# Kernel optimization log

Measured on AMD Instinct MI355X. Metric: run time of the kernel, lower is better.

## Reference

```python
import jax, jax.numpy as jnp
import numpy as np

N_NODES = 100000
D = 128


def gcn_conv(x, W, b, src, dst, deg_inv_sqrt):
    # PyG GCNConv: linear transform, symmetric-normalized aggregation with self-loops, bias
    h = x @ W  # [N, D_out]
    norm = deg_inv_sqrt[src] * deg_inv_sqrt[dst]  # [E_tot]
    msgs = h[src] * norm[:, None]  # gather + scale  [E_tot, D_out]
    out = jax.ops.segment_sum(msgs, dst, num_segments=x.shape[0])  # scatter-add to targets
    return out + b


def _prep_edges(edge_index, n_nodes):
    # add self-loops (weight 1) and compute deg^{-1/2} over targets (flow source_to_target)
    loops = jnp.arange(n_nodes, dtype=edge_index.dtype)
    src = jnp.concatenate([edge_index[0], loops])
    dst = jnp.concatenate([edge_index[1], loops])
    deg = jax.ops.segment_sum(jnp.ones_like(dst, dtype=jnp.float32), dst, num_segments=n_nodes)
    deg_inv_sqrt = jnp.where(deg > 0, jax.lax.rsqrt(jnp.maximum(deg, 1.0)), 0.0)
    return src, dst, deg_inv_sqrt


def setup_inputs() -> dict:
    key = jax.random.key(0)
    ks = jax.random.split(key, 8)
    node_fts = jax.random.normal(ks[0], (N_NODES, D), dtype=jnp.float32)
    edge_index = jax.random.randint(ks[1], (2, 1600000), 0, N_NODES, dtype=jnp.int64)
    scale = 1.0 / np.sqrt(D)
    W1 = jax.random.uniform(ks[2], (D, D), jnp.float32, -scale, scale)
    b1 = jnp.zeros((D,), jnp.float32)
    W2 = jax.random.uniform(ks[3], (D, D), jnp.float32, -scale, scale)
    b2 = jnp.zeros((D,), jnp.float32)
    W3 = jax.random.uniform(ks[4], (D, D), jnp.float32, -scale, scale)
    b3 = jnp.zeros((D,), jnp.float32)
    return {"node_fts": node_fts, "edge_index": edge_index,
            "W1": W1, "b1": b1, "W2": W2, "b2": b2, "W3": W3, "b3": b3}


def reference(node_fts, edge_index, W1, b1, W2, b2, W3, b3):
    n = node_fts.shape[0]
    src, dst, dinv = _prep_edges(edge_index, n)
    x = jax.nn.relu(gcn_conv(node_fts, W1, b1, src, dst, dinv))
    x = jax.nn.relu(gcn_conv(x, W2, b2, src, dst, dinv))
    x = jax.nn.relu(gcn_conv(x, W3, b3, src, dst, dinv))
    return x
```

## Files before the change

kernel.cpp:

```cpp
#include <hip/hip_runtime.h>

#define NN 100000
#define EE 1600000
#define NPART 8
#define PSZ (NN / NPART)
#define NI4 (EE / 4)
#define SUBW 196
#define NSB (NPART * 64)
#define SCAP 4096
#define RCAP 8192
#define LBCAP 96
#define ROWCAP 64
#define WTB 48

typedef __attribute__((ext_vector_type(8))) short bf16x8;
typedef __attribute__((ext_vector_type(4))) float f32x4;

__device__ inline unsigned int f2bf2(float a, float b) {
    unsigned int ua = __float_as_uint(a);
    unsigned int ub = __float_as_uint(b);
    ua = (ua + 0x7fffu + ((ua >> 16) & 1u)) >> 16;
    ub = (ub + 0x7fffu + ((ub >> 16) & 1u)) >> 16;
    return ua | (ub << 16);
}
__device__ inline unsigned short f2bf(float a) {
    unsigned int u = __float_as_uint(a);
    return (unsigned short)((u + 0x7fffu + ((u >> 16) & 1u)) >> 16);
}
__device__ inline float2 bf2f2(unsigned int u) {
    return make_float2(__uint_as_float(u << 16), __uint_as_float(u & 0xffff0000u));
}


__global__ __launch_bounds__(256) void fbwt_kernel(const int4* __restrict__ src4,
                                                   const int4* __restrict__ dst4,
                                                   int* __restrict__ gcur2,
                                                   uint2* __restrict__ buckets2,
                                                   const float* __restrict__ W1,
                                                   const float* __restrict__ W2,
                                                   const float* __restrict__ W3,
                                                   unsigned short* __restrict__ wt1,
                                                   unsigned short* __restrict__ wt2,
                                                   unsigned short* __restrict__ wt3,
                                                   unsigned int* __restrict__ hb,
                                                   float* __restrict__ dinv) {
    __shared__ uint2 bins[64][LBCAP];
    __shared__ int bcnt[64];
    __shared__ int gbase[64];
    __shared__ float tile[32][33];
    const int bx = blockIdx.x;

    if (bx < WTB) {
        const int m = bx >> 4;
        const int tl = bx & 15;
        const int ti = tl >> 2, tj = tl & 3;
        const float* W = m == 0 ? W1 : (m == 1 ? W2 : W3);
        unsigned short* wt = m == 0 ? wt1 : (m == 1 ? wt2 : wt3);
        const int r = threadIdx.x >> 5, c = threadIdx.x & 31;
#pragma unroll
        for (int rr = r; rr < 32; rr += 8)
            tile[rr][c] = W[(ti * 32 + rr) * 128 + tj * 32 + c];
        __syncthreads();
#pragma unroll
        for (int rr = r; rr < 32; rr += 8)
            wt[(size_t)(tj * 32 + rr) * 128 + ti * 32 + c] = f2bf(tile[c][rr]);
        if (bx == 0) {
            if (threadIdx.x < 64) hb[(size_t)NN * 64 + threadIdx.x] = 0;
            if (threadIdx.x == 64) dinv[NN] = 0.0f;
        }
        return;
    }

    const int fb = bx - WTB;
    const int p = fb >> 6;
    const int c = fb & 63;
    if (threadIdx.x < 64) bcnt[threadIdx.x] = 0;
    __syncthreads();
    const int lo = p * PSZ, hi = lo + PSZ;
    const int chunk4 = NI4 / 64;
    const int a0 = c * chunk4, a1 = a0 + chunk4;
    for (int i = a0 + threadIdx.x; i < a1; i += 256) {
        int4 d4 = dst4[i];
        bool m0 = (d4.x >= lo && d4.x < hi);
        bool m1 = (d4.y >= lo && d4.y < hi);
        bool m2 = (d4.z >= lo && d4.z < hi);
        bool m3 = (d4.w >= lo && d4.w < hi);
        if (!(m0 | m1 | m2 | m3)) continue;
        int4 s4 = src4[i];
        int ss[4] = {s4.x, s4.y, s4.z, s4.w};
        int dd[4] = {d4.x, d4.y, d4.z, d4.w};
        bool mm[4] = {m0, m1, m2, m3};
#pragma unroll
        for (int k = 0; k < 4; ++k) {
            if (!mm[k]) continue;
            int li = (dd[k] - lo) / SUBW;
            int pos = atomicAdd(&bcnt[li], 1);
            if (pos < LBCAP) {
                bins[li][pos] = make_uint2((unsigned)ss[k], (unsigned)dd[k]);
            } else {
                int sb = p * 64 + li;
                int gp = atomicAdd(&gcur2[sb], 1);
                buckets2[(size_t)sb * SCAP + gp] = make_uint2((unsigned)ss[k], (unsigned)dd[k]);
            }
        }
    }
    __syncthreads();
    if (threadIdx.x < 64) {
        int cc = min(bcnt[threadIdx.x], LBCAP);
        gbase[threadIdx.x] = atomicAdd(&gcur2[p * 64 + threadIdx.x], cc);
        bcnt[threadIdx.x] = cc;
    }
    __syncthreads();
    for (int b = 0; b < 64; ++b) {
        const int cc = bcnt[b];
        uint2* outp = buckets2 + (size_t)(p * 64 + b) * SCAP + gbase[b];
        for (int i = threadIdx.x; i < cc; i += 256) outp[i] = bins[b][i];
    }
}


template <bool F32IN>
__device__ __forceinline__ void gemm_body(int wave, const void* __restrict__ xin,
                                          const unsigned short* __restrict__ wt,
                                          unsigned int* __restrict__ hb) {
    const int base = wave * 64;
    if (base >= NN) return;
    const int lane = threadIdx.x & 63;
    const int r = lane & 15;
    const int q = lane >> 4;
    const unsigned short* wrow = wt + (size_t)r * 128 + q * 8;
    bf16x8 wfr[4][8];
#pragma unroll
    for (int kc = 0; kc < 4; ++kc)
#pragma unroll
        for (int nt = 0; nt < 8; ++nt)
            wfr[kc][nt] = *(const bf16x8*)(wrow + (size_t)nt * 16 * 128 + kc * 32);
#pragma unroll
    for (int tt = 0; tt < 4; ++tt) {
        const int m0 = base + tt * 16;
        if (m0 >= NN) break;
        f32x4 acc[8] = {};
#pragma unroll
        for (int kc = 0; kc < 4; ++kc) {
            bf16x8 xf;
            if (F32IN) {
                const float* xrow = (const float*)xin + (size_t)(m0 + r) * 128 + q * 8 + kc * 32;
                float4 a = *(const float4*)xrow;
                float4 b = *(const float4*)(xrow + 4);
                unsigned short tmp[8] = {f2bf(a.x), f2bf(a.y), f2bf(a.z), f2bf(a.w),
                                         f2bf(b.x), f2bf(b.y), f2bf(b.z), f2bf(b.w)};
                xf = *(const bf16x8*)tmp;
            } else {
                const unsigned short* xrow =
                    (const unsigned short*)xin + (size_t)(m0 + r) * 128 + q * 8 + kc * 32;
                xf = *(const bf16x8*)xrow;
            }
#pragma unroll
            for (int nt = 0; nt < 8; ++nt)
                acc[nt] = __builtin_amdgcn_mfma_f32_16x16x32_bf16(wfr[kc][nt], xf, acc[nt], 0, 0, 0);
        }
        const int orow = m0 + r;
        unsigned int* hrow = hb + (size_t)orow * 64;
#pragma unroll
        for (int nt = 0; nt < 8; ++nt) {
            int n = nt * 16 + q * 4;
            *(uint2*)(hrow + (n >> 1)) =
                make_uint2(f2bf2(acc[nt][0], acc[nt][1]), f2bf2(acc[nt][2], acc[nt][3]));
        }
    }
}


__global__ __launch_bounds__(256, 2) void sort3_gemm1_kernel(const uint2* __restrict__ buckets2,
                                                             const int* __restrict__ gcur2,
                                                             int* __restrict__ csr,
                                                             int* __restrict__ deg,
                                                             float* __restrict__ dinv,
                                                             const float* __restrict__ x0,
                                                             const unsigned short* __restrict__ wt1,
                                                             unsigned int* __restrict__ hb) {
    __shared__ int hist[256];
    __shared__ int pscan[256];
    __shared__ int lcur[256];
    __shared__ int rs[256];
    __shared__ int staged[RCAP];
    if (blockIdx.x >= 512) {
        const int wave = (blockIdx.x - 512) * 4 + (threadIdx.x >> 6);
        gemm_body<true>(wave, (const void*)x0, wt1, hb);
        return;
    }
    const int sb = blockIdx.x;
    const int li = sb & 63;
    const int base_node = (sb >> 6) * PSZ + li * SUBW;
    const int nnodes = min(SUBW, PSZ - li * SUBW);
    const int scnt = gcur2[sb];
    const uint2* bk = buckets2 + (size_t)sb * SCAP;
    const int t = threadIdx.x;
    hist[t] = 0;
    __syncthreads();
    for (int i = t; i < scnt; i += 256) atomicAdd(&hist[(int)bk[i].y - base_node], 1);
    __syncthreads();
    const int padded = (t < nnodes) ? ((hist[t] + 7) & ~7) : 0;
    pscan[t] = padded;
    __syncthreads();
    for (int off = 1; off < 256; off <<= 1) {
        int v = (t >= off) ? pscan[t - off] : 0;
        __syncthreads();
        pscan[t] += v;
        __syncthreads();
    }
    const int rstart = pscan[t] - padded;
    lcur[t] = rstart;
    rs[t] = rstart;
    __syncthreads();
    const int total = pscan[255];
    for (int i = t; i < total; i += 256) staged[i] = NN;
    __syncthreads();
    for (int i = t; i < scnt; i += 256) {
        uint2 r = bk[i];
        int pos = atomicAdd(&lcur[(int)r.y - base_node], 1);
        staged[pos] = (int)r.x;
    }
    __syncthreads();
    const int4* staged4 = (const int4*)staged;
    int4* csr4 = (int4*)csr;
    const int4 sv = make_int4(NN, NN, NN, NN);
    for (int i = t; i < nnodes * 16; i += 256) {
        const int n = i >> 4, s = i & 15;
        const int pad = (hist[n] + 7) & ~7;
        int4 v = (s * 4 < pad) ? staged4[(rs[n] >> 2) + s] : sv;
        csr4[((size_t)(base_node + n) << 4) + s] = v;
    }
    if (t < nnodes) {
        int dg = hist[t];
        deg[base_node + t] = dg;
        dinv[base_node + t] = rsqrtf(1.0f + (float)dg);
    }
}

template <bool F32IN>
__global__ __launch_bounds__(256, 2) void gemm_kernel(const void* __restrict__ xin,
                                                      const unsigned short* __restrict__ wt,
                                                      unsigned int* __restrict__ hb) {
    const int wave = blockIdx.x * 4 + (threadIdx.x >> 6);
    gemm_body<F32IN>(wave, xin, wt, hb);
}


#define GATH4(c, v0, v1, v2, v3, w0, w1, w2, w3)                              \
    unsigned int v0 = hb[(size_t)(c).x * 64 + j], v1 = hb[(size_t)(c).y * 64 + j], \
                 v2 = hb[(size_t)(c).z * 64 + j], v3 = hb[(size_t)(c).w * 64 + j]; \
    float w0 = dinv[(c).x], w1 = dinv[(c).y], w2 = dinv[(c).z], w3 = dinv[(c).w];

#define ACC4(v0, v1, v2, v3, w0, w1, w2, w3)                                  \
    {                                                                         \
        float2 f0 = bf2f2(v0), f1 = bf2f2(v1), f2 = bf2f2(v2), f3 = bf2f2(v3);\
        acc.x += (w0 * f0.x + w1 * f1.x) + (w2 * f2.x + w3 * f3.x);           \
        acc.y += (w0 * f0.y + w1 * f1.y) + (w2 * f2.y + w3 * f3.y);           \
    }

template <bool BF16OUT>
__global__ __launch_bounds__(256) void aggregate_kernel(const unsigned int* __restrict__ hb,
                                                        const int* __restrict__ csr,
                                                        const int* __restrict__ deg,
                                                        const float* __restrict__ dinv,
                                                        const float2* __restrict__ bias2,
                                                        void* __restrict__ outp) {
    const int d = blockIdx.x * 4 + (threadIdx.x >> 6);
    const int j = threadIdx.x & 63;
    const int dg = deg[d];
    const float dv = dinv[d];
    const int4* crow = (const int4*)(csr + ((size_t)d << 6));
    float2 acc;
    {
        float2 s = bf2f2(hb[(size_t)d * 64 + j]);
        acc.x = dv * s.x;
        acc.y = dv * s.y;
    }
    int4 c0 = crow[0], c1 = crow[1], c2 = crow[2], c3 = crow[3];
    int4 c4 = crow[4], c5 = crow[5], c6 = crow[6], c7 = crow[7];
    GATH4(c0, va0, va1, va2, va3, wa0, wa1, wa2, wa3)
    GATH4(c1, vb0, vb1, vb2, vb3, wb0, wb1, wb2, wb3)
    GATH4(c2, vc0, vc1, vc2, vc3, wc0, wc1, wc2, wc3)
    GATH4(c3, vd0, vd1, vd2, vd3, wd0, wd1, wd2, wd3)
    GATH4(c4, ve0, ve1, ve2, ve3, we0, we1, we2, we3)
    GATH4(c5, vf0, vf1, vf2, vf3, wf0, wf1, wf2, wf3)
    GATH4(c6, vg0, vg1, vg2, vg3, wg0, wg1, wg2, wg3)
    GATH4(c7, vh0, vh1, vh2, vh3, wh0, wh1, wh2, wh3)
    ACC4(va0, va1, va2, va3, wa0, wa1, wa2, wa3)
    ACC4(vb0, vb1, vb2, vb3, wb0, wb1, wb2, wb3)
    ACC4(vc0, vc1, vc2, vc3, wc0, wc1, wc2, wc3)
    ACC4(vd0, vd1, vd2, vd3, wd0, wd1, wd2, wd3)
    ACC4(ve0, ve1, ve2, ve3, we0, we1, we2, we3)
    ACC4(vf0, vf1, vf2, vf3, wf0, wf1, wf2, wf3)
    ACC4(vg0, vg1, vg2, vg3, wg0, wg1, wg2, wg3)
    ACC4(vh0, vh1, vh2, vh3, wh0, wh1, wh2, wh3)
    const int padded = min((dg + 7) & ~7, ROWCAP);
    for (int e = 32; e < padded; e += 8) {
        int4 t0 = crow[e >> 2], t1 = crow[(e >> 2) + 1];
        GATH4(t0, x0, x1, x2, x3, y0, y1, y2, y3)
        GATH4(t1, x4, x5, x6, x7, y4, y5, y6, y7)
        ACC4(x0, x1, x2, x3, y0, y1, y2, y3)
        ACC4(x4, x5, x6, x7, y4, y5, y6, y7)
    }
    float2 bb = bias2[j];
    float ox = fmaxf(dv * acc.x + bb.x, 0.0f);
    float oy = fmaxf(dv * acc.y + bb.y, 0.0f);
    if (BF16OUT) {
        ((unsigned int*)outp)[(size_t)d * 64 + j] = f2bf2(ox, oy);
    } else {
        ((float2*)outp)[(size_t)d * 64 + j] = make_float2(ox, oy);
    }
}


extern "C" void kernel_launch(void* const* d_in, const int* in_sizes, int n_in,
                              void* d_out, int out_size, void* d_ws, size_t ws_size,
                              hipStream_t stream) {
    const float* x0 = (const float*)d_in[0];
    const int* ei = (const int*)d_in[1];
    const float* W1 = (const float*)d_in[2];
    const float* b1 = (const float*)d_in[3];
    const float* W2 = (const float*)d_in[4];
    const float* b2 = (const float*)d_in[5];
    const float* W3 = (const float*)d_in[6];
    const float* b3 = (const float*)d_in[7];
    float* out = (float*)d_out;

    char* ws = (char*)d_ws;
    size_t off = 0;
    auto alloc = [&](size_t bytes) -> void* {
        off = (off + 511) & ~(size_t)511;
        void* p = ws + off;
        off += bytes;
        return p;
    };
    unsigned int* hb = (unsigned int*)alloc(((size_t)NN + 1) * 64 * 4);
    int* csr = (int*)alloc((size_t)NN * ROWCAP * sizeof(int));
    uint2* buckets2 = (uint2*)alloc((size_t)NSB * SCAP * sizeof(uint2));
    int* deg = (int*)alloc((size_t)NN * sizeof(int));
    float* dinv = (float*)alloc(((size_t)NN + 1) * sizeof(float));
    int* gcur2 = (int*)alloc(NSB * sizeof(int));
    unsigned short* wt1 = (unsigned short*)alloc(128 * 128 * 2);
    unsigned short* wt2 = (unsigned short*)alloc(128 * 128 * 2);
    unsigned short* wt3 = (unsigned short*)alloc(128 * 128 * 2);

    unsigned int* xact = (unsigned int*)d_out;

    const int4* src4 = (const int4*)ei;
    const int4* dst4 = (const int4*)(ei + EE);

    hipMemsetAsync(gcur2, 0, NSB * sizeof(int), stream);
    fbwt_kernel<<<WTB + 512, 256, 0, stream>>>(src4, dst4, gcur2, buckets2,
                                               W1, W2, W3, wt1, wt2, wt3, hb, dinv);
    sort3_gemm1_kernel<<<903, 256, 0, stream>>>(buckets2, gcur2, csr, deg, dinv,
                                                x0, wt1, hb);
    aggregate_kernel<true><<<NN / 4, 256, 0, stream>>>(hb, csr, deg, dinv,
                                                       (const float2*)b1, (void*)xact);
    gemm_kernel<false><<<391, 256, 0, stream>>>((const void*)xact, wt2, hb);
    aggregate_kernel<true><<<NN / 4, 256, 0, stream>>>(hb, csr, deg, dinv,
                                                       (const float2*)b2, (void*)xact);
    gemm_kernel<false><<<391, 256, 0, stream>>>((const void*)xact, wt3, hb);
    aggregate_kernel<false><<<NN / 4, 256, 0, stream>>>(hb, csr, deg, dinv,
                                                        (const float2*)b3, (void*)out);
}
```

Measured before the change: 491.5 us.

## Prescale GEMM output by source dinv and loop aggregation over padded degree

The layer-2 and layer-3 GEMMs now multiply each output row by its source node's deg^{-1/2} before writing bf16, so the matching aggregation kernels skip the per-edge dinv gather and multiply. The aggregation loop also changes from a fixed 32-entry prologue plus an 8-wide loop to a 16-wide loop over the padded degree with an 8-wide tail. This avoids reading padding slots for low-degree nodes and removes a random gather per edge. The cost is rounding the scaled values to bf16 before summation, and the loop no longer clamps at ROWCAP.

```diff
diff --git a/kernel.cpp b/kernel.cpp
--- a/kernel.cpp
+++ b/kernel.cpp
@@ -119,9 +119,10 @@
 }
 
 
-template <bool F32IN>
+template <bool F32IN, bool SCALE>
 __device__ __forceinline__ void gemm_body(int wave, const void* __restrict__ xin,
                                           const unsigned short* __restrict__ wt,
+                                          const float* __restrict__ dinv,
                                           unsigned int* __restrict__ hb) {
     const int base = wave * 64;
     if (base >= NN) return;
@@ -160,12 +161,19 @@
                 acc[nt] = __builtin_amdgcn_mfma_f32_16x16x32_bf16(wfr[kc][nt], xf, acc[nt], 0, 0, 0);
         }
         const int orow = m0 + r;
+        const float dvr = SCALE ? dinv[orow] : 1.0f;
         unsigned int* hrow = hb + (size_t)orow * 64;
 #pragma unroll
         for (int nt = 0; nt < 8; ++nt) {
             int n = nt * 16 + q * 4;
-            *(uint2*)(hrow + (n >> 1)) =
-                make_uint2(f2bf2(acc[nt][0], acc[nt][1]), f2bf2(acc[nt][2], acc[nt][3]));
+            if (SCALE) {
+                *(uint2*)(hrow + (n >> 1)) =
+                    make_uint2(f2bf2(acc[nt][0] * dvr, acc[nt][1] * dvr),
+                               f2bf2(acc[nt][2] * dvr, acc[nt][3] * dvr));
+            } else {
+                *(uint2*)(hrow + (n >> 1)) =
+                    make_uint2(f2bf2(acc[nt][0], acc[nt][1]), f2bf2(acc[nt][2], acc[nt][3]));
+            }
         }
     }
 }
@@ -186,7 +194,7 @@
     __shared__ int staged[RCAP];
     if (blockIdx.x >= 512) {
         const int wave = (blockIdx.x - 512) * 4 + (threadIdx.x >> 6);
-        gemm_body<true>(wave, (const void*)x0, wt1, hb);
+        gemm_body<true, false>(wave, (const void*)x0, wt1, nullptr, hb);
         return;
     }
     const int sb = blockIdx.x;
@@ -238,28 +246,16 @@
     }
 }
 
-template <bool F32IN>
 __global__ __launch_bounds__(256, 2) void gemm_kernel(const void* __restrict__ xin,
                                                       const unsigned short* __restrict__ wt,
+                                                      const float* __restrict__ dinv,
                                                       unsigned int* __restrict__ hb) {
     const int wave = blockIdx.x * 4 + (threadIdx.x >> 6);
-    gemm_body<F32IN>(wave, xin, wt, hb);
-}
-
-
-#define GATH4(c, v0, v1, v2, v3, w0, w1, w2, w3)                              \
-    unsigned int v0 = hb[(size_t)(c).x * 64 + j], v1 = hb[(size_t)(c).y * 64 + j], \
-                 v2 = hb[(size_t)(c).z * 64 + j], v3 = hb[(size_t)(c).w * 64 + j]; \
-    float w0 = dinv[(c).x], w1 = dinv[(c).y], w2 = dinv[(c).z], w3 = dinv[(c).w];
-
-#define ACC4(v0, v1, v2, v3, w0, w1, w2, w3)                                  \
-    {                                                                         \
-        float2 f0 = bf2f2(v0), f1 = bf2f2(v1), f2 = bf2f2(v2), f3 = bf2f2(v3);\
-        acc.x += (w0 * f0.x + w1 * f1.x) + (w2 * f2.x + w3 * f3.x);           \
-        acc.y += (w0 * f0.y + w1 * f1.y) + (w2 * f2.y + w3 * f3.y);           \
-    }
-
-template <bool BF16OUT>
+    gemm_body<false, true>(wave, xin, wt, dinv, hb);
+}
+
+
+template <bool BF16OUT, bool WEIGHTED>
 __global__ __launch_bounds__(256) void aggregate_kernel(const unsigned int* __restrict__ hb,
                                                         const int* __restrict__ csr,
                                                         const int* __restrict__ deg,
@@ -270,38 +266,83 @@
     const int j = threadIdx.x & 63;
     const int dg = deg[d];
     const float dv = dinv[d];
-    const int4* crow = (const int4*)(csr + ((size_t)d << 6));
+    int e = d << 6;
+    const int end = e + ((dg + 7) & ~7);
     float2 acc;
     {
         float2 s = bf2f2(hb[(size_t)d * 64 + j]);
-        acc.x = dv * s.x;
-        acc.y = dv * s.y;
-    }
-    int4 c0 = crow[0], c1 = crow[1], c2 = crow[2], c3 = crow[3];
-    int4 c4 = crow[4], c5 = crow[5], c6 = crow[6], c7 = crow[7];
-    GATH4(c0, va0, va1, va2, va3, wa0, wa1, wa2, wa3)
-    GATH4(c1, vb0, vb1, vb2, vb3, wb0, wb1, wb2, wb3)
-    GATH4(c2, vc0, vc1, vc2, vc3, wc0, wc1, wc2, wc3)
-    GATH4(c3, vd0, vd1, vd2, vd3, wd0, wd1, wd2, wd3)
-    GATH4(c4, ve0, ve1, ve2, ve3, we0, we1, we2, we3)
-    GATH4(c5, vf0, vf1, vf2, vf3, wf0, wf1, wf2, wf3)
-    GATH4(c6, vg0, vg1, vg2, vg3, wg0, wg1, wg2, wg3)
-    GATH4(c7, vh0, vh1, vh2, vh3, wh0, wh1, wh2, wh3)
-    ACC4(va0, va1, va2, va3, wa0, wa1, wa2, wa3)
-    ACC4(vb0, vb1, vb2, vb3, wb0, wb1, wb2, wb3)
-    ACC4(vc0, vc1, vc2, vc3, wc0, wc1, wc2, wc3)
-    ACC4(vd0, vd1, vd2, vd3, wd0, wd1, wd2, wd3)
-    ACC4(ve0, ve1, ve2, ve3, we0, we1, we2, we3)
-    ACC4(vf0, vf1, vf2, vf3, wf0, wf1, wf2, wf3)
-    ACC4(vg0, vg1, vg2, vg3, wg0, wg1, wg2, wg3)
-    ACC4(vh0, vh1, vh2, vh3, wh0, wh1, wh2, wh3)
-    const int padded = min((dg + 7) & ~7, ROWCAP);
-    for (int e = 32; e < padded; e += 8) {
-        int4 t0 = crow[e >> 2], t1 = crow[(e >> 2) + 1];
-        GATH4(t0, x0, x1, x2, x3, y0, y1, y2, y3)
-        GATH4(t1, x4, x5, x6, x7, y4, y5, y6, y7)
-        ACC4(x0, x1, x2, x3, y0, y1, y2, y3)
-        ACC4(x4, x5, x6, x7, y4, y5, y6, y7)
+        if (WEIGHTED) { acc.x = dv * s.x; acc.y = dv * s.y; }
+        else          { acc.x = s.x;      acc.y = s.y; }
+    }
+    for (; e + 16 <= end; e += 16) {
+        int4 c0 = *(const int4*)(csr + e);
+        int4 c1 = *(const int4*)(csr + e + 4);
+        int4 c2 = *(const int4*)(csr + e + 8);
+        int4 c3 = *(const int4*)(csr + e + 12);
+        unsigned int v0 = hb[(size_t)c0.x * 64 + j];
+        unsigned int v1 = hb[(size_t)c0.y * 64 + j];
+        unsigned int v2 = hb[(size_t)c0.z * 64 + j];
+        unsigned int v3 = hb[(size_t)c0.w * 64 + j];
+        unsigned int v4 = hb[(size_t)c1.x * 64 + j];
+        unsigned int v5 = hb[(size_t)c1.y * 64 + j];
+        unsigned int v6 = hb[(size_t)c1.z * 64 + j];
+        unsigned int v7 = hb[(size_t)c1.w * 64 + j];
+        unsigned int v8 = hb[(size_t)c2.x * 64 + j];
+        unsigned int v9 = hb[(size_t)c2.y * 64 + j];
+        unsigned int va = hb[(size_t)c2.z * 64 + j];
+        unsigned int vb = hb[(size_t)c2.w * 64 + j];
+        unsigned int vc = hb[(size_t)c3.x * 64 + j];
+        unsigned int vd = hb[(size_t)c3.y * 64 + j];
+        unsigned int ve = hb[(size_t)c3.z * 64 + j];
+        unsigned int vf = hb[(size_t)c3.w * 64 + j];
+        float2 f0 = bf2f2(v0), f1 = bf2f2(v1), f2 = bf2f2(v2), f3 = bf2f2(v3);
+        float2 f4 = bf2f2(v4), f5 = bf2f2(v5), f6 = bf2f2(v6), f7 = bf2f2(v7);
+        float2 f8 = bf2f2(v8), f9 = bf2f2(v9), fa = bf2f2(va), fb = bf2f2(vb);
+        float2 fc = bf2f2(vc), fd = bf2f2(vd), fe = bf2f2(ve), ff = bf2f2(vf);
+        if (WEIGHTED) {
+            float w0 = dinv[c0.x], w1 = dinv[c0.y], w2 = dinv[c0.z], w3 = dinv[c0.w];
+            float w4 = dinv[c1.x], w5 = dinv[c1.y], w6 = dinv[c1.z], w7 = dinv[c1.w];
+            float w8 = dinv[c2.x], w9 = dinv[c2.y], wa = dinv[c2.z], wb = dinv[c2.w];
+            float wc = dinv[c3.x], wd = dinv[c3.y], we = dinv[c3.z], wf = dinv[c3.w];
+            acc.x += ((w0 * f0.x + w1 * f1.x) + (w2 * f2.x + w3 * f3.x)) +
+                     ((w4 * f4.x + w5 * f5.x) + (w6 * f6.x + w7 * f7.x)) +
+                     ((w8 * f8.x + w9 * f9.x) + (wa * fa.x + wb * fb.x)) +
+                     ((wc * fc.x + wd * fd.x) + (we * fe.x + wf * ff.x));
+            acc.y += ((w0 * f0.y + w1 * f1.y) + (w2 * f2.y + w3 * f3.y)) +
+                     ((w4 * f4.y + w5 * f5.y) + (w6 * f6.y + w7 * f7.y)) +
+                     ((w8 * f8.y + w9 * f9.y) + (wa * fa.y + wb * fb.y)) +
+                     ((wc * fc.y + wd * fd.y) + (we * fe.y + wf * ff.y));
+        } else {
+            acc.x += ((f0.x + f1.x) + (f2.x + f3.x)) + ((f4.x + f5.x) + (f6.x + f7.x)) +
+                     ((f8.x + f9.x) + (fa.x + fb.x)) + ((fc.x + fd.x) + (fe.x + ff.x));
+            acc.y += ((f0.y + f1.y) + (f2.y + f3.y)) + ((f4.y + f5.y) + (f6.y + f7.y)) +
+                     ((f8.y + f9.y) + (fa.y + fb.y)) + ((fc.y + fd.y) + (fe.y + ff.y));
+        }
+    }
+    if (e < end) {
+        int4 c0 = *(const int4*)(csr + e);
+        int4 c1 = *(const int4*)(csr + e + 4);
+        unsigned int v0 = hb[(size_t)c0.x * 64 + j];
+        unsigned int v1 = hb[(size_t)c0.y * 64 + j];
+        unsigned int v2 = hb[(size_t)c0.z * 64 + j];
+        unsigned int v3 = hb[(size_t)c0.w * 64 + j];
+        unsigned int v4 = hb[(size_t)c1.x * 64 + j];
+        unsigned int v5 = hb[(size_t)c1.y * 64 + j];
+        unsigned int v6 = hb[(size_t)c1.z * 64 + j];
+        unsigned int v7 = hb[(size_t)c1.w * 64 + j];
+        float2 f0 = bf2f2(v0), f1 = bf2f2(v1), f2 = bf2f2(v2), f3 = bf2f2(v3);
+        float2 f4 = bf2f2(v4), f5 = bf2f2(v5), f6 = bf2f2(v6), f7 = bf2f2(v7);
+        if (WEIGHTED) {
+            float w0 = dinv[c0.x], w1 = dinv[c0.y], w2 = dinv[c0.z], w3 = dinv[c0.w];
+            float w4 = dinv[c1.x], w5 = dinv[c1.y], w6 = dinv[c1.z], w7 = dinv[c1.w];
+            acc.x += ((w0 * f0.x + w1 * f1.x) + (w2 * f2.x + w3 * f3.x)) +
+                     ((w4 * f4.x + w5 * f5.x) + (w6 * f6.x + w7 * f7.x));
+            acc.y += ((w0 * f0.y + w1 * f1.y) + (w2 * f2.y + w3 * f3.y)) +
+                     ((w4 * f4.y + w5 * f5.y) + (w6 * f6.y + w7 * f7.y));
+        } else {
+            acc.x += ((f0.x + f1.x) + (f2.x + f3.x)) + ((f4.x + f5.x) + (f6.x + f7.x));
+            acc.y += ((f0.y + f1.y) + (f2.y + f3.y)) + ((f4.y + f5.y) + (f6.y + f7.y));
+        }
     }
     float2 bb = bias2[j];
     float ox = fmaxf(dv * acc.x + bb.x, 0.0f);
@@ -355,12 +396,12 @@
                                                W1, W2, W3, wt1, wt2, wt3, hb, dinv);
     sort3_gemm1_kernel<<<903, 256, 0, stream>>>(buckets2, gcur2, csr, deg, dinv,
                                                 x0, wt1, hb);
-    aggregate_kernel<true><<<NN / 4, 256, 0, stream>>>(hb, csr, deg, dinv,
-                                                       (const float2*)b1, (void*)xact);
-    gemm_kernel<false><<<391, 256, 0, stream>>>((const void*)xact, wt2, hb);
-    aggregate_kernel<true><<<NN / 4, 256, 0, stream>>>(hb, csr, deg, dinv,
-                                                       (const float2*)b2, (void*)xact);
-    gemm_kernel<false><<<391, 256, 0, stream>>>((const void*)xact, wt3, hb);
-    aggregate_kernel<false><<<NN / 4, 256, 0, stream>>>(hb, csr, deg, dinv,
-                                                        (const float2*)b3, (void*)out);
-}
+    aggregate_kernel<true, true><<<NN / 4, 256, 0, stream>>>(hb, csr, deg, dinv,
+                                                             (const float2*)b1, (void*)xact);
+    gemm_kernel<<<391, 256, 0, stream>>>((const void*)xact, wt2, dinv, hb);
+    aggregate_kernel<true, false><<<NN / 4, 256, 0, stream>>>(hb, csr, deg, dinv,
+                                                              (const float2*)b2, (void*)xact);
+    gemm_kernel<<<391, 256, 0, stream>>>((const void*)xact, wt3, dinv, hb);
+    aggregate_kernel<false, false><<<NN / 4, 256, 0, stream>>>(hb, csr, deg, dinv,
+                                                               (const float2*)b3, (void*)out);
+}
```

Measured after the change: 411.5 us. -16.3%, faster.
